# Optimization experiments

Hardware: AMD Instinct MI355X
Metric: run time of the kernel (lower is better)

## Reference

```python
import jax, jax.numpy as jnp
import numpy as np

N, E, IN, H, D, C = 30000, 400000, 128, 4, 64, 40
EPS = 1e-5
SLOPE = 0.2  # DGL GATv2Conv leaky_relu negative_slope default


def setup_inputs() -> dict:
    key = jax.random.key(0)
    ks = jax.random.split(key, 20)
    def rn(k, shape, s=0.05):
        return jax.random.normal(k, shape, jnp.float32) * s
    return {
        "x": jax.random.normal(ks[0], (N, IN), jnp.float32),
        "src": jax.random.randint(ks[1], (E,), 0, N),
        "dst": jax.random.randint(ks[2], (E,), 0, N),
        # layer 0: in=128 -> heads*64 (residual projection since 128 != 256)
        "W_src0": rn(ks[3], (IN, H * D)), "W_dst0": rn(ks[4], (IN, H * D)),
        "b0": jnp.zeros((H * D,), jnp.float32), "attn0": rn(ks[5], (H, D)),
        "res_W0": rn(ks[6], (IN, H * D)),
        # layer 1: 256 -> heads*64 (identity residual since 256 == 256)
        "W_src1": rn(ks[7], (H * D, H * D)), "W_dst1": rn(ks[8], (H * D, H * D)),
        "b1": jnp.zeros((H * D,), jnp.float32), "attn1": rn(ks[9], (H, D)),
        # layer 2: 256 -> heads*40 (residual projection)
        "W_src2": rn(ks[10], (H * D, H * C)), "W_dst2": rn(ks[11], (H * D, H * C)),
        "b2": jnp.zeros((H * C,), jnp.float32), "attn2": rn(ks[12], (H, C)),
        "res_W2": rn(ks[13], (H * D, H * C)),
        # batchnorm affine params (training-mode batch stats)
        "g0": jnp.ones((H * D,), jnp.float32), "be0": jnp.zeros((H * D,), jnp.float32),
        "g1": jnp.ones((H * D,), jnp.float32), "be1": jnp.zeros((H * D,), jnp.float32),
    }


def gatv2_layer(h, src, dst, Wsrc, Wdst, b, attn, resW, out_dim, relu_act):
    # DGL GATv2Conv: score_e = attn . leaky_relu(fc_src(h)[u] + fc_dst(h)[v])
    n = h.shape[0]
    fs = (h @ Wsrc).reshape(n, H, out_dim)
    fd = (h @ Wdst).reshape(n, H, out_dim)
    e = jax.nn.leaky_relu(fs[src] + fd[dst], SLOPE)      # [E, H, out]
    score = jnp.einsum("ehd,hd->eh", e, attn)            # [E, H]
    # segment softmax over incoming edges of each dst node
    m = jax.ops.segment_max(score, dst, num_segments=n)
    m = jnp.where(jnp.isfinite(m), m, 0.0)               # zero in-degree safety
    ex = jnp.exp(score - m[dst])
    denom = jax.ops.segment_sum(ex, dst, num_segments=n)
    alpha = ex / jnp.maximum(denom, 1e-9)[dst]
    rst = jax.ops.segment_sum(alpha[:, :, None] * fs[src], dst, num_segments=n)
    res = (h @ resW).reshape(n, H, out_dim) if resW is not None else h.reshape(n, H, out_dim)
    rst = rst + res + b.reshape(1, H, out_dim)
    return jax.nn.relu(rst) if relu_act else rst


def batchnorm(h, g, be):
    mu = h.mean(0)
    var = h.var(0)  # biased variance, as torch BN uses for normalization
    return g * (h - mu) * jax.lax.rsqrt(var + EPS) + be


def reference(x, src, dst, W_src0, W_dst0, b0, attn0, res_W0, W_src1, W_dst1, b1, attn1, W_src2, W_dst2, b2, attn2, res_W2, g0, be0, g1, be1):
    h = gatv2_layer(x, src, dst, W_src0, W_dst0, b0, attn0, res_W0, D, True)
    h = jax.nn.relu(batchnorm(h.reshape(N, H * D), g0, be0))  # dropout = identity (eval)
    h = gatv2_layer(h, src, dst, W_src1, W_dst1, b1, attn1, None, D, True)
    h = jax.nn.relu(batchnorm(h.reshape(N, H * D), g1, be1))
    h = gatv2_layer(h, src, dst, W_src2, W_dst2, b2, attn2, res_W2, C, False)
    h = h.mean(1)  # mean over heads -> [N, C]
    return jax.nn.log_softmax(h, axis=-1)
```

## Files before the change

### kernel.cpp

```cpp
#include <hip/hip_runtime.h>
#include <hip/hip_bf16.h>
#include <math.h>

#define NN 30000
#define EE 400000
#define INP 128
#define HH 4
#define DD 64
#define CC 40
#define HD 256
#define HC 160
#define NBLK 118

typedef unsigned short ushort;
typedef __attribute__((ext_vector_type(8))) short s8v;
typedef __attribute__((ext_vector_type(4))) float f4v;
typedef __attribute__((ext_vector_type(2))) float f2;


__device__ inline ushort bf16_of_float(float f) {
    __hip_bfloat16 b = __float2bfloat16(f);
    return *(ushort*)&b;
}
__device__ __forceinline__ float b2f(ushort u) { return __uint_as_float(((unsigned)u) << 16); }

__device__ __forceinline__ f2 cvt2v(unsigned d) {
    f2 r;
    r.x = __uint_as_float(d << 16);
    r.y = __uint_as_float(d & 0xFFFF0000u);
    return r;
}
__device__ __forceinline__ f2 splat2(float s) { f2 r = {s, s}; return r; }
__device__ __forceinline__ f2 f2fmav(f2 a, f2 b, f2 c) {
#if __has_builtin(__builtin_elementwise_fma)
    return __builtin_elementwise_fma(a, b, c);
#else
    f2 r; r.x = __fmaf_rn(a.x, b.x, c.x); r.y = __fmaf_rn(a.y, b.y, c.y); return r;
#endif
}
__device__ __forceinline__ f2 f2maxv(f2 a, f2 b) {
#if __has_builtin(__builtin_elementwise_max)
    return __builtin_elementwise_max(a, b);
#else
    f2 r; r.x = fmaxf(a.x, b.x); r.y = fmaxf(a.y, b.y); return r;
#endif
}

__device__ __forceinline__ void gld16(const void* g, void* l) {
    __builtin_amdgcn_global_load_lds((const __attribute__((address_space(1))) void*)g,
                                     (__attribute__((address_space(3))) void*)l, 16, 0, 0);
}

__device__ __forceinline__ float rowsum16(float x) {
    int t;
    t = __builtin_amdgcn_update_dpp(0, __float_as_int(x), 0x128, 0xF, 0xF, false); x += __int_as_float(t);
    t = __builtin_amdgcn_update_dpp(0, __float_as_int(x), 0x124, 0xF, 0xF, false); x += __int_as_float(t);
    t = __builtin_amdgcn_update_dpp(0, __float_as_int(x), 0x122, 0xF, 0xF, false); x += __int_as_float(t);
    t = __builtin_amdgcn_update_dpp(0, __float_as_int(x), 0x121, 0xF, 0xF, false); x += __int_as_float(t);
    return x;
}
__device__ __forceinline__ float rowmax16(float x) {
    int t;
    t = __builtin_amdgcn_update_dpp(0, __float_as_int(x), 0x128, 0xF, 0xF, false); x = fmaxf(x, __int_as_float(t));
    t = __builtin_amdgcn_update_dpp(0, __float_as_int(x), 0x124, 0xF, 0xF, false); x = fmaxf(x, __int_as_float(t));
    t = __builtin_amdgcn_update_dpp(0, __float_as_int(x), 0x122, 0xF, 0xF, false); x = fmaxf(x, __int_as_float(t));
    t = __builtin_amdgcn_update_dpp(0, __float_as_int(x), 0x121, 0xF, 0xF, false); x = fmaxf(x, __int_as_float(t));
    return x;
}

#define XB 3750
#define TB 1408
#define ZB 240

__global__ __launch_bounds__(256) void k_prep(const float* __restrict__ x, ushort* __restrict__ xc,
        const float* W0, const float* W1, const float* W2, const float* W3,
        const float* W4, const float* W5, const float* W6, const float* W7,
        ushort* bt0, ushort* bt1, ushort* bt2,
        int* __restrict__ zero_region,
        const float* b0, const float* a0, const float* b1, const float* a1,
        const float* b2, const float* a2, const float* g0, const float* be0,
        const float* g1, const float* be1, ushort* __restrict__ smallv) {
    int b = blockIdx.x, t = threadIdx.x;
    if (b < XB) {
        int i = b * 256 + t;
        if (i < NN * INP / 4) {
            float4 v = ((const float4*)x)[i];
            ushort4 o;
            o.x = bf16_of_float(v.x); o.y = bf16_of_float(v.y);
            o.z = bf16_of_float(v.z); o.w = bf16_of_float(v.w);
            ((ushort4*)xc)[i] = o;
        }
    } else if (b < XB + TB) {
        const float* Ws[8] = {W0, W1, W2, W3, W4, W5, W6, W7};
        int g = (b - XB) * 256 + t;
        if (g < 98304) {
            int seg = g >> 15, local = g & 32767;
            int n = local >> 7, k = local & 127;
            bt0[g] = bf16_of_float(Ws[seg][k * 256 + n]);
        } else if (g < 229376) {
            int gg = g - 98304;
            int seg = gg >> 16, local = gg & 65535;
            int n = local >> 8, k = local & 255;
            bt1[gg] = bf16_of_float(Ws[3 + seg][k * 256 + n]);
        } else if (g < 360448) {
            int gg = g - 229376;
            int n = gg >> 8, k = gg & 255;
            ushort val = 0;
            if (n < 480) {
                int seg = n / 160;
                int nn = n - seg * 160;
                val = bf16_of_float(Ws[5 + seg][k * 160 + nn]);
            }
            bt2[gg] = val;
        }
    } else if (b < XB + TB + ZB) {
        int i = (b - XB - TB) * 256 + t;
        if (i < 1024 + 2 * NN + 192) zero_region[i] = 0;
    } else {
        const float* ptrs[10] = {b0, a0, b1, a1, b2, a2, g0, be0, g1, be1};
        const int sz[10] = {256, 256, 256, 256, 160, 160, 256, 256, 256, 256};
        int off = 0;
        for (int j = 0; j < 10; j++) {
            if (t < sz[j]) smallv[off + t] = bf16_of_float(ptrs[j][t]);
            off += sz[j];
        }
    }
}


__global__ __launch_bounds__(256) void k_hist(const int* __restrict__ dst, int* __restrict__ cnt) {
    int e = blockIdx.x * 256 + threadIdx.x;
    if (e < EE) atomicAdd(&cnt[dst[e]], 1);
}

__global__ __launch_bounds__(256) void k_binbeg(const int* __restrict__ cnt, int* __restrict__ binCnt,
                                                int* __restrict__ beg, int* __restrict__ total) {
    __shared__ int lb[64];
    __shared__ int ss[256];
    __shared__ int base;
    int t = threadIdx.x;
    if (t < 64) lb[t] = 0;
    __syncthreads();
    int i = blockIdx.x * 256 + t;
    int c = (i < NN) ? cnt[i] : 0;
    int rc = (c + 3) & ~3;
    if (i < NN) atomicAdd(&lb[63 - min(c, 63)], 1);
    ss[t] = rc;
    __syncthreads();
    if (t < 64 && lb[t] > 0) atomicAdd(&binCnt[t], lb[t]);
    for (int o = 1; o < 256; o <<= 1) {
        int v = (t >= o) ? ss[t - o] : 0;
        __syncthreads();
        ss[t] += v;
        __syncthreads();
    }
    if (t == 255) base = atomicAdd(total, ss[255]);
    __syncthreads();
    if (i < NN) beg[i] = base + ss[t] - rc;
}

__global__ __launch_bounds__(256) void k_orderscatter(const int* __restrict__ cnt, const int* __restrict__ binCnt,
                                                      int* __restrict__ binPos, int* __restrict__ order,
                                                      const int* __restrict__ src, const int* __restrict__ dst,
                                                      const int* __restrict__ beg, int* __restrict__ pos,
                                                      int* __restrict__ srcs) {
    int t = threadIdx.x;
    if (blockIdx.x < NBLK) {
        __shared__ int lb[64], lbase[64], bpre[64];
        if (t < 64) { lb[t] = 0; bpre[t] = binCnt[t]; }
        __syncthreads();
        int i = blockIdx.x * 256 + t;
        int bin = 0, rank = 0;
        if (i < NN) {
            bin = 63 - min(cnt[i], 63);
            rank = atomicAdd(&lb[bin], 1);
        }
        for (int o = 1; o < 64; o <<= 1) {
            int v = (t >= o && t < 64) ? bpre[t - o] : 0;
            __syncthreads();
            if (t < 64) bpre[t] += v;
            __syncthreads();
        }
        if (t < 64 && lb[t] > 0)
            lbase[t] = bpre[t] - binCnt[t] + atomicAdd(&binPos[t], lb[t]);
        __syncthreads();
        if (i < NN) order[lbase[bin] + rank] = i;
    } else {
        int e = (blockIdx.x - NBLK) * 256 + t;
        if (e < EE) {
            int d = dst[e];
            int p = atomicAdd(&pos[d], 1);
            srcs[beg[d] + p] = src[e];
        }
    }
}


template<int K, int SEGW, int NSEG>
__global__ __launch_bounds__(256) void k_gemm_tiled(const ushort* __restrict__ A,
                                                    const ushort* __restrict__ Bt,
                                                    ushort* __restrict__ o0, ushort* __restrict__ o1,
                                                    ushort* __restrict__ o2) {
    __shared__ ushort As[128 * 32];
    __shared__ ushort Bs[128 * 32];
    int t = threadIdx.x;
    int wave = t >> 6, lane = t & 63;
    int m = lane & 15, q = lane >> 4;
    int row0 = blockIdx.x * 128, col0 = blockIdx.y * 128;
    int wr = (wave >> 1) << 6, wc = (wave & 1) << 6;
    f4v acc[4][4] = {};
    int c1 = t, c2 = t + 256;
    int ar1 = min(row0 + (c1 >> 2), NN - 1);
    int ar2 = min(row0 + (c2 >> 2), NN - 1);
    const ushort* a1 = A + (size_t)ar1 * K + (c1 & 3) * 8;
    const ushort* a2 = A + (size_t)ar2 * K + (c2 & 3) * 8;
    const ushort* b1 = Bt + (size_t)(col0 + (c1 >> 2)) * K + (c1 & 3) * 8;
    const ushort* b2 = Bt + (size_t)(col0 + (c2 >> 2)) * K + (c2 & 3) * 8;
    int wbase = wave << 10;
    char* AsB = (char*)As;
    char* BsB = (char*)Bs;

#pragma unroll
    for (int kt = 0; kt < K; kt += 32) {
        __syncthreads();
        gld16(a1 + kt, AsB + wbase);
        gld16(a2 + kt, AsB + 4096 + wbase);
        gld16(b1 + kt, BsB + wbase);
        gld16(b2 + kt, BsB + 4096 + wbase);
        __syncthreads();
        s8v af[4], bg[4];
#pragma unroll
        for (int i = 0; i < 4; i++) af[i] = *(const s8v*)&As[(wr + i * 16 + m) * 32 + q * 8];
#pragma unroll
        for (int c = 0; c < 4; c++) bg[c] = *(const s8v*)&Bs[(wc + c * 16 + m) * 32 + q * 8];
#pragma unroll
        for (int i = 0; i < 4; i++)
#pragma unroll
            for (int c = 0; c < 4; c++)
                acc[i][c] = __builtin_amdgcn_mfma_f32_16x16x32_bf16(bg[c], af[i], acc[i][c], 0, 0, 0);
    }

#pragma unroll
    for (int c = 0; c < 4; c++) {
        int gcb = col0 + wc + c * 16;
        if (gcb < SEGW * NSEG) {
            int seg = gcb / SEGW;
            int colb = gcb - seg * SEGW + q * 4;
            ushort* op = seg == 0 ? o0 : (seg == 1 ? o1 : o2);
#pragma unroll
            for (int i = 0; i < 4; i++) {
                int gr = row0 + wr + i * 16 + m;
                if (gr < NN) {
                    ushort4 s4;
                    s4.x = bf16_of_float(acc[i][c][0]);
                    s4.y = bf16_of_float(acc[i][c][1]);
                    s4.z = bf16_of_float(acc[i][c][2]);
                    s4.w = bf16_of_float(acc[i][c][3]);
                    *(ushort4*)&op[(size_t)gr * SEGW + colb] = s4;
                }
            }
        }
    }
}


template<int DH, bool FINAL>
__global__ __launch_bounds__(256) void k_aggregate(const ushort* __restrict__ fs, const ushort* __restrict__ fd,
                                                   const ushort* __restrict__ res,
                                                   const ushort* __restrict__ attn,
                                                   const ushort* __restrict__ bias,
                                                   const int* __restrict__ beg, const int* __restrict__ cnt,
                                                   const int* __restrict__ srcs,
                                                   const int* __restrict__ order,
                                                   ushort* __restrict__ outb, float* __restrict__ outf) {
    constexpr int F = HH * DH;
    constexpr int JMAX = DH >> 2;
    int tt = threadIdx.x;
    int v = __builtin_amdgcn_readfirstlane(order[blockIdx.x * 4 + (tt >> 6)]);
    int lane = tt & 63;
    int h = lane >> 4, j = lane & 15;
    bool act = j < JMAX;
    unsigned off = h * DH + 4 * j;
    unsigned vbase = (unsigned)v * F + off;
    f2 fda = {0.f, 0.f}, fdb = {0.f, 0.f}, ava = {0.f, 0.f}, avb = {0.f, 0.f};
    if (act) {
        uint2 d = *(const uint2*)&fd[vbase];
        fda = cvt2v(d.x); fdb = cvt2v(d.y);
        uint2 a = *(const uint2*)&attn[off];
        const float LOG2E = 1.4426950408889634f;
        ava = cvt2v(a.x) * LOG2E; avb = cvt2v(a.y) * LOG2E;
    }
    float l = 0.f;
    f2 acca = {0.f, 0.f}, accb = {0.f, 0.f};
    int b0i = beg[v], end = b0i + cnt[v];

    auto ldrow = [&](int u, f2& ra, f2& rb) {
        ra = splat2(0.f); rb = splat2(0.f);
        if (act) {
            uint2 d = *(const uint2*)&fs[(unsigned)u * F + off];
            ra = cvt2v(d.x); rb = cvt2v(d.y);
        }
    };
    auto dotlr = [&](const f2& ra, const f2& rb) -> float {
        f2 t0 = ra + fda;
        f2 t1 = rb + fdb;
        t0 = f2maxv(t0, t0 * 0.2f);
        t1 = f2maxv(t1, t1 * 0.2f);
        f2 p2 = ava * t0;
        p2 = f2fmav(avb, t1, p2);
        return p2.x + p2.y;
    };
    auto quadc = [&](const f2& r0a, const f2& r0b, const f2& r1a, const f2& r1b,
                     const f2& r2a, const f2& r2b, const f2& r3a, const f2& r3b) {
        float p0 = rowsum16(dotlr(r0a, r0b));
        float p1 = rowsum16(dotlr(r1a, r1b));
        float p2 = rowsum16(dotlr(r2a, r2b));
        float p3 = rowsum16(dotlr(r3a, r3b));
        float w0 = exp2f(p0), w1 = exp2f(p1), w2 = exp2f(p2), w3 = exp2f(p3);
        l += (w0 + w1) + (w2 + w3);
        acca = f2fmav(splat2(w0), r0a, acca);
        accb = f2fmav(splat2(w0), r0b, accb);
        acca = f2fmav(splat2(w1), r1a, acca);
        accb = f2fmav(splat2(w1), r1b, accb);
        acca = f2fmav(splat2(w2), r2a, acca);
        accb = f2fmav(splat2(w2), r2b, accb);
        acca = f2fmav(splat2(w3), r3a, acca);
        accb = f2fmav(splat2(w3), r3b, accb);
    };

    int i = b0i;
    if (i + 3 < end) {
        int4 u = *(const int4*)&srcs[i];
        f2 r0a, r0b, r1a, r1b, r2a, r2b, r3a, r3b;
        ldrow(u.x, r0a, r0b); ldrow(u.y, r1a, r1b);
        ldrow(u.z, r2a, r2b); ldrow(u.w, r3a, r3b);
        int4 un = (i + 7 < end) ? *(const int4*)&srcs[i + 4] : u;
        for (i += 4; i + 3 < end; i += 4) {
            f2 s0a, s0b, s1a, s1b, s2a, s2b, s3a, s3b;
            ldrow(un.x, s0a, s0b); ldrow(un.y, s1a, s1b);
            ldrow(un.z, s2a, s2b); ldrow(un.w, s3a, s3b);
            if (i + 7 < end) un = *(const int4*)&srcs[i + 4];
            __builtin_amdgcn_sched_barrier(0);
            quadc(r0a, r0b, r1a, r1b, r2a, r2b, r3a, r3b);
            r0a = s0a; r0b = s0b; r1a = s1a; r1b = s1b;
            r2a = s2a; r2b = s2b; r3a = s3a; r3b = s3b;
        }
        quadc(r0a, r0b, r1a, r1b, r2a, r2b, r3a, r3b);
    }
    for (; i < end; i++) {
        f2 ra, rb;
        ldrow(srcs[i], ra, rb);
        float p0 = rowsum16(dotlr(ra, rb));
        float w0 = exp2f(p0);
        l += w0;
        acca = f2fmav(splat2(w0), ra, acca);
        accb = f2fmav(splat2(w0), rb, accb);
    }

    float4 o4 = {0.f, 0.f, 0.f, 0.f};
    if (act) {
        float inv = 1.f / fmaxf(l, 1e-9f);
        uint2 rr = *(const uint2*)&res[vbase];
        f2 rl = cvt2v(rr.x), rh = cvt2v(rr.y);
        uint2 bb = *(const uint2*)&bias[off];
        f2 bl = cvt2v(bb.x), bh = cvt2v(bb.y);
        o4.x = acca.x * inv + rl.x + bl.x;
        o4.y = acca.y * inv + rl.y + bl.y;
        o4.z = accb.x * inv + rh.x + bh.x;
        o4.w = accb.y * inv + rh.y + bh.y;
        if (!FINAL) {
            o4.x = fmaxf(o4.x, 0.f); o4.y = fmaxf(o4.y, 0.f);
            o4.z = fmaxf(o4.z, 0.f); o4.w = fmaxf(o4.w, 0.f);
        }
    }
    if (!FINAL) {
        if (act) {
            ushort4 s4;
            s4.x = bf16_of_float(o4.x); s4.y = bf16_of_float(o4.y);
            s4.z = bf16_of_float(o4.z); s4.w = bf16_of_float(o4.w);
            *(ushort4*)&outb[vbase] = s4;
        }
    } else {
#pragma unroll
        for (int msk = 16; msk <= 32; msk <<= 1) {
            o4.x += __shfl_xor(o4.x, msk, 64);
            o4.y += __shfl_xor(o4.y, msk, 64);
            o4.z += __shfl_xor(o4.z, msk, 64);
            o4.w += __shfl_xor(o4.w, msk, 64);
        }
        float4 zv = make_float4(0.25f * o4.x, 0.25f * o4.y, 0.25f * o4.z, 0.25f * o4.w);
        float mx4 = act ? fmaxf(fmaxf(zv.x, zv.y), fmaxf(zv.z, zv.w)) : -1e30f;
        float mx = rowmax16(mx4);
        float es = 0.f;
        if (act) es = __expf(zv.x - mx) + __expf(zv.y - mx) + __expf(zv.z - mx) + __expf(zv.w - mx);
        float ssum = rowsum16(es);
        float lse = mx + logf(ssum);
        if (act && h == 0) {
            float4 w4 = make_float4(zv.x - lse, zv.y - lse, zv.z - lse, zv.w - lse);
            *(float4*)&outf[(size_t)v * CC + 4 * j] = w4;
        }
    }
}


__global__ __launch_bounds__(256) void k_bn_partial(const ushort* __restrict__ h, float* __restrict__ sum,
                                                    float* __restrict__ sumsq) {
    int c = threadIdx.x;
    int r0 = blockIdx.x * 128;
    int r1 = min(NN, r0 + 128);
    float s0 = 0.f, ss0 = 0.f, s1 = 0.f, ss1 = 0.f;
    int r = r0;
#pragma unroll 4
    for (; r + 1 < r1; r += 2) {
        float v0 = b2f(h[(size_t)r * HD + c]);
        float v1 = b2f(h[(size_t)(r + 1) * HD + c]);
        s0 += v0; ss0 = __fmaf_rn(v0, v0, ss0);
        s1 += v1; ss1 = __fmaf_rn(v1, v1, ss1);
    }
    if (r < r1) {
        float v0 = b2f(h[(size_t)r * HD + c]);
        s0 += v0; ss0 = __fmaf_rn(v0, v0, ss0);
    }
    atomicAdd(&sum[c], s0 + s1);
    atomicAdd(&sumsq[c], ss0 + ss1);
}


__global__ __launch_bounds__(256) void k_bn_norm(const ushort* __restrict__ hin, const float* __restrict__ sum,
                                                 const float* __restrict__ sumsq,
                                                 const ushort* __restrict__ g,
                                                 const ushort* __restrict__ be,
                                                 ushort* __restrict__ hbf) {
    int i4 = blockIdx.x * 256 + threadIdx.x;
    if (i4 < NN * HD / 4) {
        int base = i4 * 4;
        int c = base & (HD - 1);
        ushort4 hv = ((const ushort4*)hin)[i4];
        ushort4 ov;
        float vv[4] = {b2f(hv.x), b2f(hv.y), b2f(hv.z), b2f(hv.w)};
        ushort* po = (ushort*)&ov;
#pragma unroll
        for (int k = 0; k < 4; k++) {
            float mean = sum[c + k] * (1.0f / NN);
            float var = fmaxf(sumsq[c + k] * (1.0f / NN) - mean * mean, 0.f);
            float y = b2f(g[c + k]) * (vv[k] - mean) * rsqrtf(var + 1e-5f) + b2f(be[c + k]);
            po[k] = bf16_of_float(fmaxf(y, 0.f));
        }
        ((ushort4*)hbf)[i4] = ov;
    }
}


static inline char* alignup(char* p) { return (char*)(((size_t)p + 255) & ~(size_t)255); }

extern "C" void kernel_launch(void* const* d_in, const int* in_sizes, int n_in,
                              void* d_out, int out_size, void* d_ws, size_t ws_size,
                              hipStream_t stream) {
    const float* x     = (const float*)d_in[0];
    const int*  src    = (const int*)d_in[1];
    const int*  dst    = (const int*)d_in[2];
    const float* Wsrc0 = (const float*)d_in[3];
    const float* Wdst0 = (const float*)d_in[4];
    const float* b0    = (const float*)d_in[5];
    const float* attn0 = (const float*)d_in[6];
    const float* resW0 = (const float*)d_in[7];
    const float* Wsrc1 = (const float*)d_in[8];
    const float* Wdst1 = (const float*)d_in[9];
    const float* b1    = (const float*)d_in[10];
    const float* attn1 = (const float*)d_in[11];
    const float* Wsrc2 = (const float*)d_in[12];
    const float* Wdst2 = (const float*)d_in[13];
    const float* b2    = (const float*)d_in[14];
    const float* attn2 = (const float*)d_in[15];
    const float* resW2 = (const float*)d_in[16];
    const float* g0    = (const float*)d_in[17];
    const float* be0   = (const float*)d_in[18];
    const float* g1    = (const float*)d_in[19];
    const float* be1   = (const float*)d_in[20];

    char* w = (char*)d_ws;
    const size_t NF = (size_t)NN * HD;
    ushort* fsb = (ushort*)w; w += NF * 2;
    ushort* fdb = (ushort*)w; w += NF * 2;
    ushort* resb= (ushort*)w; w += NF * 2;
    ushort* hag = (ushort*)w; w += NF * 2;
    ushort* hbf = (ushort*)w; w += NF * 2;
    ushort* xc  = (ushort*)w; w += (size_t)NN * INP * 2;
    ushort* bt0 = (ushort*)w; w += 768 * 128 * 2;
    ushort* bt1 = (ushort*)w; w += 512 * 256 * 2;
    ushort* bt2 = (ushort*)w; w += 512 * 256 * 2;
    ushort* smallv = (ushort*)w; w += 2368 * 2; w = alignup(w);
    float* bnstats = (float*)w; w += 1024 * 4;
    int* cnt    = (int*)w; w += NN * 4;
    int* pos    = (int*)w; w += NN * 4;
    int* binCnt = (int*)w; w += 64 * 4;
    int* binPos = (int*)w; w += 64 * 4;
    int* total  = (int*)w; w += 64 * 4; w = alignup(w);
    int* beg    = (int*)w; w += NN * 4; w = alignup(w);
    int* order  = (int*)w; w += NN * 4; w = alignup(w);
    int* srcs   = (int*)w; w += (size_t)(EE + 3 * NN + 64) * 4;

    const ushort* c_b0    = smallv + 0;
    const ushort* c_attn0 = smallv + 256;
    const ushort* c_b1    = smallv + 512;
    const ushort* c_attn1 = smallv + 768;
    const ushort* c_b2    = smallv + 1024;
    const ushort* c_attn2 = smallv + 1184;
    const ushort* c_g0    = smallv + 1344;
    const ushort* c_be0   = smallv + 1600;
    const ushort* c_g1    = smallv + 1856;
    const ushort* c_be1   = smallv + 2112;

    k_prep<<<XB + TB + ZB + 1, 256, 0, stream>>>(x, xc,
        Wsrc0, Wdst0, resW0, Wsrc1, Wdst1, Wsrc2, Wdst2, resW2, bt0, bt1, bt2,
        (int*)bnstats,
        b0, attn0, b1, attn1, b2, attn2, g0, be0, g1, be1, smallv);

    k_hist<<<(EE + 255) / 256, 256, 0, stream>>>(dst, cnt);
    k_binbeg<<<NBLK, 256, 0, stream>>>(cnt, binCnt, beg, total);
    k_orderscatter<<<NBLK + (EE + 255) / 256, 256, 0, stream>>>(cnt, binCnt, binPos, order,
                                                                src, dst, beg, pos, srcs);

    const int MB = (NN + 127) / 128;

    k_gemm_tiled<128, 256, 3><<<dim3(MB, 6), 256, 0, stream>>>(xc, bt0, fsb, fdb, resb);
    k_aggregate<DD, false><<<NN / 4, 256, 0, stream>>>(fsb, fdb, resb, c_attn0, c_b0,
        beg, cnt, srcs, order, hag, nullptr);
    k_bn_partial<<<MB, 256, 0, stream>>>(hag, bnstats, bnstats + 256);
    k_bn_norm<<<(int)((NF / 4 + 255) / 256), 256, 0, stream>>>(hag, bnstats, bnstats + 256,
                                                               c_g0, c_be0, hbf);

    k_gemm_tiled<256, 256, 2><<<dim3(MB, 4), 256, 0, stream>>>(hbf, bt1, fsb, fdb, nullptr);
    k_aggregate<DD, false><<<NN / 4, 256, 0, stream>>>(fsb, fdb, hbf, c_attn1, c_b1,
        beg, cnt, srcs, order, hag, nullptr);
    k_bn_partial<<<MB, 256, 0, stream>>>(hag, bnstats + 512, bnstats + 768);
    k_bn_norm<<<(int)((NF / 4 + 255) / 256), 256, 0, stream>>>(hag, bnstats + 512, bnstats + 768,
                                                               c_g1, c_be1, hbf);

    k_gemm_tiled<256, 160, 3><<<dim3(MB, 4), 256, 0, stream>>>(hbf, bt2, fsb, fdb, resb);
    k_aggregate<CC, true><<<NN / 4, 256, 0, stream>>>(fsb, fdb, resb, c_attn2, c_b2,
        beg, cnt, srcs, order, nullptr, (float*)d_out);
}
```

Measured before the change: 361.2 us.

## Add XCD-aware GEMM tile swizzle, packed-f32 asm and ping-pong edge pipeline

Remaps GEMM workgroup IDs so consecutive tiles land on the same XCD, which should improve L2 reuse across the eight chiplets. The aggregation kernel switches to inline-asm v_pk_add/mul/fma_f32 and the raw hardware exp2 builtin, dropping the range-checking wrapper. The edge loop becomes a two-buffer ping-pong (A/B quads), which removes the per-iteration register copies. Inline asm limits the compiler's scheduling, and the raw exp2 can behave differently on denormals.

```diff
diff --git a/kernel.cpp b/kernel.cpp
--- a/kernel.cpp
+++ b/kernel.cpp
@@ -31,12 +31,15 @@
     return r;
 }
 __device__ __forceinline__ f2 splat2(float s) { f2 r = {s, s}; return r; }
-__device__ __forceinline__ f2 f2fmav(f2 a, f2 b, f2 c) {
-#if __has_builtin(__builtin_elementwise_fma)
-    return __builtin_elementwise_fma(a, b, c);
-#else
-    f2 r; r.x = __fmaf_rn(a.x, b.x, c.x); r.y = __fmaf_rn(a.y, b.y, c.y); return r;
-#endif
+
+__device__ __forceinline__ f2 pk_add(f2 a, f2 b) {
+    f2 d; asm("v_pk_add_f32 %0, %1, %2" : "=v"(d) : "v"(a), "v"(b)); return d;
+}
+__device__ __forceinline__ f2 pk_mul(f2 a, f2 b) {
+    f2 d; asm("v_pk_mul_f32 %0, %1, %2" : "=v"(d) : "v"(a), "v"(b)); return d;
+}
+__device__ __forceinline__ f2 pk_fma(f2 a, f2 b, f2 c) {
+    f2 d; asm("v_pk_fma_f32 %0, %1, %2, %3" : "=v"(d) : "v"(a), "v"(b), "v"(c)); return d;
 }
 __device__ __forceinline__ f2 f2maxv(f2 a, f2 b) {
 #if __has_builtin(__builtin_elementwise_max)
@@ -206,7 +209,16 @@
     int t = threadIdx.x;
     int wave = t >> 6, lane = t & 63;
     int m = lane & 15, q = lane >> 4;
-    int row0 = blockIdx.x * 128, col0 = blockIdx.y * 128;
+
+    int nwg = gridDim.x * gridDim.y;
+    int NB = gridDim.y;
+    int ld = blockIdx.x + gridDim.x * blockIdx.y;
+    int xcd = ld & 7, pos = ld >> 3;
+    int qq = nwg >> 3, rr = nwg & 7;
+    int base = (xcd < rr) ? xcd * (qq + 1) : rr * (qq + 1) + (xcd - rr) * qq;
+    int swz = base + pos;
+    int row0 = (swz / NB) * 128, col0 = (swz % NB) * 128;
+
     int wr = (wave >> 1) << 6, wc = (wave & 1) << 6;
     f4v acc[4][4] = {};
     int c1 = t, c2 = t + 256;
@@ -290,9 +302,12 @@
         const float LOG2E = 1.4426950408889634f;
         ava = cvt2v(a.x) * LOG2E; avb = cvt2v(a.y) * LOG2E;
     }
+    const f2 c02 = {0.2f, 0.2f};
     float l = 0.f;
     f2 acca = {0.f, 0.f}, accb = {0.f, 0.f};
     int b0i = beg[v], end = b0i + cnt[v];
+
+    struct Q8 { f2 a0, b0, a1, b1, a2, b2, a3, b3; };
 
     auto ldrow = [&](int u, f2& ra, f2& rb) {
         ra = splat2(0.f); rb = splat2(0.f);
@@ -301,60 +316,71 @@
             ra = cvt2v(d.x); rb = cvt2v(d.y);
         }
     };
+    auto ldq = [&](int4 u, Q8& r) {
+        ldrow(u.x, r.a0, r.b0); ldrow(u.y, r.a1, r.b1);
+        ldrow(u.z, r.a2, r.b2); ldrow(u.w, r.a3, r.b3);
+    };
     auto dotlr = [&](const f2& ra, const f2& rb) -> float {
-        f2 t0 = ra + fda;
-        f2 t1 = rb + fdb;
-        t0 = f2maxv(t0, t0 * 0.2f);
-        t1 = f2maxv(t1, t1 * 0.2f);
-        f2 p2 = ava * t0;
-        p2 = f2fmav(avb, t1, p2);
-        return p2.x + p2.y;
+        f2 t0 = pk_add(ra, fda);
+        f2 t1 = pk_add(rb, fdb);
+        t0 = f2maxv(t0, pk_mul(t0, c02));
+        t1 = f2maxv(t1, pk_mul(t1, c02));
+        f2 p = pk_mul(ava, t0);
+        p = pk_fma(avb, t1, p);
+        return p.x + p.y;
     };
-    auto quadc = [&](const f2& r0a, const f2& r0b, const f2& r1a, const f2& r1b,
-                     const f2& r2a, const f2& r2b, const f2& r3a, const f2& r3b) {
-        float p0 = rowsum16(dotlr(r0a, r0b));
-        float p1 = rowsum16(dotlr(r1a, r1b));
-        float p2 = rowsum16(dotlr(r2a, r2b));
-        float p3 = rowsum16(dotlr(r3a, r3b));
-        float w0 = exp2f(p0), w1 = exp2f(p1), w2 = exp2f(p2), w3 = exp2f(p3);
+    auto quadc = [&](const Q8& r) {
+        float p0 = rowsum16(dotlr(r.a0, r.b0));
+        float p1 = rowsum16(dotlr(r.a1, r.b1));
+        float p2 = rowsum16(dotlr(r.a2, r.b2));
+        float p3 = rowsum16(dotlr(r.a3, r.b3));
+        float w0 = __builtin_amdgcn_exp2f(p0), w1 = __builtin_amdgcn_exp2f(p1);
+        float w2 = __builtin_amdgcn_exp2f(p2), w3 = __builtin_amdgcn_exp2f(p3);
         l += (w0 + w1) + (w2 + w3);
-        acca = f2fmav(splat2(w0), r0a, acca);
-        accb = f2fmav(splat2(w0), r0b, accb);
-        acca = f2fmav(splat2(w1), r1a, acca);
-        accb = f2fmav(splat2(w1), r1b, accb);
-        acca = f2fmav(splat2(w2), r2a, acca);
-        accb = f2fmav(splat2(w2), r2b, accb);
-        acca = f2fmav(splat2(w3), r3a, acca);
-        accb = f2fmav(splat2(w3), r3b, accb);
+        f2 s0 = splat2(w0), s1 = splat2(w1), s2 = splat2(w2), s3 = splat2(w3);
+        acca = pk_fma(s0, r.a0, acca); accb = pk_fma(s0, r.b0, accb);
+        acca = pk_fma(s1, r.a1, acca); accb = pk_fma(s1, r.b1, accb);
+        acca = pk_fma(s2, r.a2, acca); accb = pk_fma(s2, r.b2, accb);
+        acca = pk_fma(s3, r.a3, acca); accb = pk_fma(s3, r.b3, accb);
     };
 
     int i = b0i;
-    if (i + 3 < end) {
+    int nfull = (end - b0i) >> 2;
+    if (nfull > 0) {
+        Q8 A, B;
         int4 u = *(const int4*)&srcs[i];
-        f2 r0a, r0b, r1a, r1b, r2a, r2b, r3a, r3b;
-        ldrow(u.x, r0a, r0b); ldrow(u.y, r1a, r1b);
-        ldrow(u.z, r2a, r2b); ldrow(u.w, r3a, r3b);
-        int4 un = (i + 7 < end) ? *(const int4*)&srcs[i + 4] : u;
-        for (i += 4; i + 3 < end; i += 4) {
-            f2 s0a, s0b, s1a, s1b, s2a, s2b, s3a, s3b;
-            ldrow(un.x, s0a, s0b); ldrow(un.y, s1a, s1b);
-            ldrow(un.z, s2a, s2b); ldrow(un.w, s3a, s3b);
-            if (i + 7 < end) un = *(const int4*)&srcs[i + 4];
+        ldq(u, A);
+        int4 un = (nfull > 1) ? *(const int4*)&srcs[i + 4] : u;
+        int q = 1;
+        for (; q + 1 < nfull; q += 2) {
+            ldq(un, B);
+            un = *(const int4*)&srcs[i + (q + 1) * 4];
             __builtin_amdgcn_sched_barrier(0);
-            quadc(r0a, r0b, r1a, r1b, r2a, r2b, r3a, r3b);
-            r0a = s0a; r0b = s0b; r1a = s1a; r1b = s1b;
-            r2a = s2a; r2b = s2b; r3a = s3a; r3b = s3b;
-        }
-        quadc(r0a, r0b, r1a, r1b, r2a, r2b, r3a, r3b);
+            quadc(A);
+            ldq(un, A);
+            if (q + 2 < nfull) un = *(const int4*)&srcs[i + (q + 2) * 4];
+            __builtin_amdgcn_sched_barrier(0);
+            quadc(B);
+        }
+        if (q < nfull) {
+            ldq(un, B);
+            __builtin_amdgcn_sched_barrier(0);
+            quadc(A);
+            quadc(B);
+        } else {
+            quadc(A);
+        }
+        i += nfull * 4;
     }
     for (; i < end; i++) {
         f2 ra, rb;
         ldrow(srcs[i], ra, rb);
         float p0 = rowsum16(dotlr(ra, rb));
-        float w0 = exp2f(p0);
+        float w0 = __builtin_amdgcn_exp2f(p0);
         l += w0;
-        acca = f2fmav(splat2(w0), ra, acca);
-        accb = f2fmav(splat2(w0), rb, accb);
+        f2 s0 = splat2(w0);
+        acca = pk_fma(s0, ra, acca);
+        accb = pk_fma(s0, rb, accb);
     }
 
     float4 o4 = {0.f, 0.f, 0.f, 0.f};
```

Result: no change. 354.3 us (-1.9%).
